# Performance work log

Measured on AMD Instinct MI355X. Metric: run time of the kernel, lower is better.

## Reference

```python
import jax, jax.numpy as jnp
import numpy as np

EMBED_DIM = 1024
HEAD_DIM = 64


def setup_inputs() -> dict:
    key = jax.random.key(0)
    ks = jax.random.split(key, 7)
    s_in = EMBED_DIM ** -0.5  # torch Linear default init scale
    x = jax.random.normal(ks[0], (4, 4096, EMBED_DIM), dtype=jnp.float32)
    Wk = jax.random.uniform(ks[1], (HEAD_DIM, EMBED_DIM), jnp.float32, -s_in, s_in)
    bk = jax.random.uniform(ks[2], (HEAD_DIM,), jnp.float32, -s_in, s_in)
    Wq = jax.random.uniform(ks[3], (HEAD_DIM, EMBED_DIM), jnp.float32, -s_in, s_in)
    bq = jax.random.uniform(ks[4], (HEAD_DIM,), jnp.float32, -s_in, s_in)
    Wv = jax.random.uniform(ks[5], (HEAD_DIM, EMBED_DIM), jnp.float32, -s_in, s_in)
    bv = jax.random.uniform(ks[6], (HEAD_DIM,), jnp.float32, -s_in, s_in)
    return {"x": x, "Wq": Wq, "bq": bq, "Wk": Wk, "bk": bk, "Wv": Wv, "bv": bv}


def reference(x, Wq, bq, Wk, bk, Wv, bv):
    # torch Linear: y = x @ W.T + b
    q = jnp.einsum('btc,dc->btd', x, Wq) + bq  # [B,T,D]
    k = jnp.einsum('btc,dc->btd', x, Wk) + bk
    v = jnp.einsum('btc,dc->btd', x, Wv) + bv
    scale = HEAD_DIM ** -0.5
    # NOTE: original divides by scale (multiplies by sqrt(head_dim)) -- faithful
    scores = jnp.einsum('btd,bsd->bts', q, k) / scale  # [B,T,T]
    attn_weights = jax.nn.softmax(scores, axis=-1)
    return jnp.einsum('bts,bsd->btd', attn_weights, v)
```

## Files before the change

kernel.cpp:

```cpp
#include <hip/hip_runtime.h>

#define BATCH 4
#define SEQ   4096
#define CDIM  1024
#define DDIM  64
#define NROW  (BATCH * SEQ)
#define SPA   70
#define NSPL  8

typedef _Float16 f16;
typedef _Float16 f16x8 __attribute__((ext_vector_type(8)));
typedef _Float16 f16x4 __attribute__((ext_vector_type(4)));
typedef __fp16   h16x2 __attribute__((ext_vector_type(2)));
typedef float    f32x4 __attribute__((ext_vector_type(4)));

#define MFMA32(a, b, c) __builtin_amdgcn_mfma_f32_16x16x32_f16((a), (b), (c), 0, 0, 0)
#define MFMA16(a, b, c) __builtin_amdgcn_mfma_f32_16x16x16f16((a), (b), (c), 0, 0, 0)

#define GLDS(g, l)                                                            \
  __builtin_amdgcn_global_load_lds((const __attribute__((address_space(1))) void*)(g), \
                                   (__attribute__((address_space(3))) void*)(l), 16, 0, 0)

#define QSCALE 11.5415603f

__device__ inline f16x8 cvt8(f32x4 a, f32x4 b) {
  h16x2 p0 = __builtin_amdgcn_cvt_pkrtz(a[0], a[1]);
  h16x2 p1 = __builtin_amdgcn_cvt_pkrtz(a[2], a[3]);
  h16x2 p2 = __builtin_amdgcn_cvt_pkrtz(b[0], b[1]);
  h16x2 p3 = __builtin_amdgcn_cvt_pkrtz(b[2], b[3]);
  f16x8 r;
  r[0] = p0[0]; r[1] = p0[1]; r[2] = p1[0]; r[3] = p1[1];
  r[4] = p2[0]; r[5] = p2[1]; r[6] = p3[0]; r[7] = p3[1];
  return r;
}

__device__ inline f16x4 cvt4(float a, float b, float c, float d) {
  h16x2 lo = __builtin_amdgcn_cvt_pkrtz(a, b);
  h16x2 hi = __builtin_amdgcn_cvt_pkrtz(c, d);
  f16x4 r;
  r[0] = lo[0]; r[1] = lo[1]; r[2] = hi[0]; r[3] = hi[1];
  return r;
}

__global__ __launch_bounds__(256) void prep_w_kernel(const float* __restrict__ Wq,
                                                     const float* __restrict__ Wk,
                                                     const float* __restrict__ Wv,
                                                     f16* __restrict__ wf2) {
  const int t = blockIdx.x * 256 + threadIdx.x;
  const int lane = t & 63;
  const int s = t >> 6;
  const int mt = s % 12, ck = s / 12;
  const int mat = mt >> 2, tile = mt & 3;
  const int n = lane & 15, quad = lane >> 4;
  const float* W = (mat == 0) ? Wq : (mat == 1) ? Wk : Wv;
  const float* src = W + (size_t)(tile * 16 + n) * CDIM + ck * 32 + quad * 8;
  const f32x4 a = *(const f32x4*)src;
  const f32x4 b = *(const f32x4*)(src + 4);
  *(f16x8*)(wf2 + (size_t)t * 8) = cvt8(a, b);
}

__global__ __launch_bounds__(256, 2) void proj_kernel(const float* __restrict__ x,
                                                      const f16* __restrict__ wf2,
                                                      const float* __restrict__ bq,
                                                      const float* __restrict__ bk,
                                                      const float* __restrict__ bv,
                                                      f16* __restrict__ qs,
                                                      f16* __restrict__ ks,
                                                      f16* __restrict__ vT) {
  __shared__ __attribute__((aligned(16))) char smem[2 * 16384];
  const int tid = threadIdx.x, lane = tid & 63, w = tid >> 6;
  const int n = lane & 15, quad = lane >> 4;
  const int rowbase = blockIdx.x * 32;

  const float* xsl = x + (size_t)(rowbase + w * 8 + (lane >> 3)) * CDIM + (lane & 7) * 4;
  const f16* wsl[3];
#pragma unroll
  for (int i = 0; i < 3; ++i)
    wsl[i] = wf2 + (size_t)(w * 3 + i) * 512 + lane * 8;

  f32x4 acc[2][3];
#pragma unroll
  for (int g = 0; g < 2; ++g)
#pragma unroll
    for (int i = 0; i < 3; ++i) acc[g][i] = (f32x4){0.f, 0.f, 0.f, 0.f};

  auto issue = [&](int ck, int b) {
    char* base = smem + b * 16384;
    GLDS(xsl + ck * 32, base + w * 1024);
#pragma unroll
    for (int i = 0; i < 3; ++i)
      GLDS(wsl[i] + (size_t)ck * 12 * 512, base + 4096 + (w * 3 + i) * 1024);
  };

  issue(0, 0);
  __syncthreads();
  for (int ck = 0; ck < 32; ++ck) {
    const int b = ck & 1;
    if (ck + 1 < 32) issue(ck + 1, b ^ 1);
    const float* xb = (const float*)(smem + b * 16384);
    const f16* wb = (const f16*)(smem + b * 16384 + 4096);
    f16x8 a[2];
#pragma unroll
    for (int g = 0; g < 2; ++g) {
      const f32x4 x0 = *(const f32x4*)(xb + (g * 16 + n) * 32 + quad * 8);
      const f32x4 x1 = *(const f32x4*)(xb + (g * 16 + n) * 32 + quad * 8 + 4);
      a[g] = cvt8(x0, x1);
    }
#pragma unroll
    for (int i = 0; i < 3; ++i) {
      const f16x8 bf = *(const f16x8*)(wb + (w * 3 + i) * 512 + lane * 8);
      acc[0][i] = MFMA32(a[0], bf, acc[0][i]);
      acc[1][i] = MFMA32(a[1], bf, acc[1][i]);
    }
    __syncthreads();
  }

  const float* bias_p[3] = {bq, bk, bv};
#pragma unroll
  for (int i = 0; i < 3; ++i) {
    const int mt = w * 3 + i;
    const int mat = mt >> 2, tile = mt & 3;
    const int d = tile * 16 + n;
    const float bias = bias_p[mat][d];
#pragma unroll
    for (int g = 0; g < 2; ++g) {
      const int r0 = rowbase + g * 16 + quad * 4;
      f32x4 aa = acc[g][i];
      if (mat == 0) {
#pragma unroll
        for (int r = 0; r < 4; ++r)
          qs[(size_t)(r0 + r) * DDIM + d] = (f16)((aa[r] + bias) * QSCALE);
      } else if (mat == 1) {
#pragma unroll
        for (int r = 0; r < 4; ++r)
          ks[(size_t)(r0 + r) * DDIM + d] = (f16)(aa[r] + bias);
      } else {
        const int bb = r0 >> 12;
        const int t = r0 & (SEQ - 1);
        *(f16x4*)(vT + (size_t)(bb * 64 + d) * SEQ + t) =
            cvt4(aa[0] + bias, aa[1] + bias, aa[2] + bias, aa[3] + bias);
      }
    }
  }
}

template <int NSPLIT>
__global__ __launch_bounds__(256, 4) void attn_kernel(const f16* __restrict__ qs,
                                                      const f16* __restrict__ ks,
                                                      const f16* __restrict__ vT,
                                                      float* __restrict__ outp,
                                                      f16* __restrict__ pacc,
                                                      float* __restrict__ pm,
                                                      float* __restrict__ pl) {
  __shared__ __attribute__((aligned(16))) f16 lk[64][SPA];
  __shared__ __attribute__((aligned(16))) f16 lv[64][SPA];
  const int tid = threadIdx.x, lane = tid & 63, w = tid >> 6;
  const int n = lane & 15, quad = lane >> 4;
  const int split = blockIdx.x % NSPLIT;
  const int rowblk = blockIdx.x / NSPLIT;
  const int row0 = rowblk * 128 + w * 32;
  const int bb = row0 >> 12;
  const int kbase = split * (SEQ / NSPLIT);
  const int NC = SEQ / NSPLIT / 64;

  const f16* kb = ks + (size_t)bb * SEQ * DDIM;
  const f16* vb = vT + (size_t)bb * DDIM * SEQ;

  const int srow = tid >> 2;
  const int scol = (tid & 3) * 16;
  const f16* kgp = kb + (size_t)(kbase + srow) * DDIM + scol;
  const f16* vgp = vb + (size_t)srow * SEQ + kbase + scol;

  f16x8 qf[2][2];
#pragma unroll
  for (int g = 0; g < 2; ++g)
#pragma unroll
    for (int hh = 0; hh < 2; ++hh)
      qf[g][hh] = *(const f16x8*)(qs + (size_t)(row0 + g * 16 + n) * DDIM + hh * 32 + quad * 8);

  f32x4 acc[2][4];
  float m[2] = {-1e30f, -1e30f}, ll[2] = {0.f, 0.f};
#pragma unroll
  for (int g = 0; g < 2; ++g)
#pragma unroll
    for (int t = 0; t < 4; ++t) acc[g][t] = (f32x4){0.f, 0.f, 0.f, 0.f};

  f16x8 kr0, kr1, vr0, vr1;
  auto gload = [&](int c) {
    const f16* kp = kgp + (size_t)c * 64 * DDIM;
    kr0 = *(const f16x8*)kp;
    kr1 = *(const f16x8*)(kp + 8);
    const f16* vp = vgp + c * 64;
    vr0 = *(const f16x8*)vp;
    vr1 = *(const f16x8*)(vp + 8);
  };

  gload(0);
  for (int c = 0; c < NC; ++c) {
    *(f16x8*)&lk[srow][scol] = kr0;
    *(f16x8*)&lk[srow][scol + 8] = kr1;
    *(f16x8*)&lv[srow][scol] = vr0;
    *(f16x8*)&lv[srow][scol + 8] = vr1;
    __syncthreads();
    if (c + 1 < NC) gload(c + 1);

    f32x4 s[2][4];
#pragma unroll
    for (int st = 0; st < 4; ++st) {
      const f16x8 klo = *(const f16x8*)&lk[st * 16 + n][quad * 8];
      const f16x8 khi = *(const f16x8*)&lk[st * 16 + n][32 + quad * 8];
#pragma unroll
      for (int g = 0; g < 2; ++g) {
        f32x4 z = (f32x4){0.f, 0.f, 0.f, 0.f};
        z = MFMA32(klo, qf[g][0], z);
        s[g][st] = MFMA32(khi, qf[g][1], z);
      }
    }

    f16x4 pq[2][4];
#pragma unroll
    for (int g = 0; g < 2; ++g) {
      f32x4 mx;
#pragma unroll
      for (int r = 0; r < 4; ++r)
        mx[r] = fmaxf(fmaxf(s[g][0][r], s[g][1][r]), fmaxf(s[g][2][r], s[g][3][r]));
      float mloc = fmaxf(fmaxf(mx[0], mx[1]), fmaxf(mx[2], mx[3]));
      mloc = fmaxf(mloc, __shfl_xor(mloc, 16));
      mloc = fmaxf(mloc, __shfl_xor(mloc, 32));
      const float mnew = fmaxf(m[g], mloc);
      const float alpha = __builtin_amdgcn_exp2f(m[g] - mnew);
      m[g] = mnew;
      float psum = 0.f;
#pragma unroll
      for (int st = 0; st < 4; ++st) {
        f32x4 p;
#pragma unroll
        for (int r = 0; r < 4; ++r) p[r] = __builtin_amdgcn_exp2f(s[g][st][r] - mnew);
        psum += (p[0] + p[1]) + (p[2] + p[3]);
        pq[g][st] = cvt4(p[0], p[1], p[2], p[3]);
      }
      ll[g] = ll[g] * alpha + psum;
#pragma unroll
      for (int t = 0; t < 4; ++t) acc[g][t] *= alpha;
    }

#pragma unroll
    for (int t = 0; t < 4; ++t)
#pragma unroll
      for (int st = 0; st < 4; ++st) {
        const f16x4 va = *(const f16x4*)&lv[t * 16 + n][st * 16 + quad * 4];
        acc[0][t] = MFMA16(va, pq[0][st], acc[0][t]);
        acc[1][t] = MFMA16(va, pq[1][st], acc[1][t]);
      }
    __syncthreads();
  }

  float lred[2];
#pragma unroll
  for (int g = 0; g < 2; ++g) {
    float l = ll[g];
    l += __shfl_xor(l, 16);
    l += __shfl_xor(l, 32);
    lred[g] = l;
  }

  if (NSPLIT == 1) {
#pragma unroll
    for (int g = 0; g < 2; ++g) {
      const float inv = 1.0f / lred[g];
      const int q = row0 + g * 16 + n;
#pragma unroll
      for (int t = 0; t < 4; ++t) {
        f32x4 o = acc[g][t];
#pragma unroll
        for (int r = 0; r < 4; ++r) o[r] *= inv;
        *(f32x4*)(outp + (size_t)q * DDIM + t * 16 + quad * 4) = o;
      }
    }
  } else {
#pragma unroll
    for (int g = 0; g < 2; ++g) {
      const int q = row0 + g * 16 + n;
#pragma unroll
      for (int t = 0; t < 4; ++t)
        *(f16x4*)(pacc + ((size_t)split * NROW + q) * DDIM + t * 16 + quad * 4) =
            cvt4(acc[g][t][0], acc[g][t][1], acc[g][t][2], acc[g][t][3]);
      if (quad == 0) {
        pm[split * NROW + q] = m[g];
        pl[split * NROW + q] = lred[g];
      }
    }
  }
}

template <int NSPLIT>
__global__ __launch_bounds__(256) void combine_kernel(const f16* __restrict__ pacc,
                                                      const float* __restrict__ pm,
                                                      const float* __restrict__ pl,
                                                      float* __restrict__ out) {
  const int idx = blockIdx.x * 256 + threadIdx.x;
  const int row = idx >> 4;
  const int c = (idx & 15) * 4;
  float mm = pm[row];
#pragma unroll
  for (int s = 1; s < NSPLIT; ++s) mm = fmaxf(mm, pm[s * NROW + row]);
  float L = 0.f;
  f32x4 o = (f32x4){0.f, 0.f, 0.f, 0.f};
#pragma unroll
  for (int s = 0; s < NSPLIT; ++s) {
    const float e = __builtin_amdgcn_exp2f(pm[s * NROW + row] - mm);
    L += pl[s * NROW + row] * e;
    const f16x4 a = *(const f16x4*)(pacc + ((size_t)s * NROW + row) * DDIM + c);
#pragma unroll
    for (int j = 0; j < 4; ++j) o[j] += (float)a[j] * e;
  }
  const float inv = 1.0f / L;
#pragma unroll
  for (int j = 0; j < 4; ++j) o[j] *= inv;
  *(f32x4*)(out + (size_t)row * DDIM + c) = o;
}

extern "C" void kernel_launch(void* const* d_in, const int* in_sizes, int n_in,
                              void* d_out, int out_size, void* d_ws, size_t ws_size,
                              hipStream_t stream) {
  const float* x  = (const float*)d_in[0];
  const float* Wq = (const float*)d_in[1];
  const float* bq = (const float*)d_in[2];
  const float* Wk = (const float*)d_in[3];
  const float* bk = (const float*)d_in[4];
  const float* Wv = (const float*)d_in[5];
  const float* bv = (const float*)d_in[6];
  float* out = (float*)d_out;

  f16* wf2 = (f16*)d_ws;
  f16* qs = wf2 + 3 * 65536;
  f16* ks = qs + (size_t)NROW * DDIM;
  f16* vT = ks + (size_t)NROW * DDIM;
  f16* pacc = vT + (size_t)NROW * DDIM;
  float* pm = (float*)(pacc + (size_t)NSPL * NROW * DDIM);
  float* pl = pm + (size_t)NSPL * NROW;
  const size_t need = (size_t)((char*)(pl + (size_t)NSPL * NROW) - (char*)d_ws);

  prep_w_kernel<<<dim3(96), dim3(256), 0, stream>>>(Wq, Wk, Wv, wf2);
  proj_kernel<<<dim3(512), dim3(256), 0, stream>>>(x, wf2, bq, bk, bv, qs, ks, vT);

  if (ws_size >= need) {
    attn_kernel<NSPL><<<dim3(128 * NSPL), dim3(256), 0, stream>>>(qs, ks, vT, nullptr, pacc, pm, pl);
    combine_kernel<NSPL><<<dim3(NROW * 16 / 256), dim3(256), 0, stream>>>(pacc, pm, pl, out);
  } else {
    attn_kernel<1><<<dim3(128), dim3(256), 0, stream>>>(qs, ks, vT, out, nullptr, nullptr, nullptr);
  }
}
```

Before: 164.7 us.

## Swizzle K/V layouts and use async global-to-LDS double buffering in attention

The projection kernel now writes K with an XOR-swizzled column layout and V into per-64-key chunked, swizzled tiles, so the attention kernel can copy them straight into LDS with global_load_lds. It double-buffers the LDS tiles, drops the padded register-staged copy and one barrier per iteration, and reads through matching swizzles to avoid bank conflicts. The projection kernel also moves to 512 threads, with each wave doing one 16-row group and separate waves loading x versus weights. Together these raise LDS usage and rely on correct swizzle and index arithmetic across both kernels.

```diff
diff --git a/kernel.cpp b/kernel.cpp
--- a/kernel.cpp
+++ b/kernel.cpp
@@ -5,7 +5,6 @@
 #define CDIM  1024
 #define DDIM  64
 #define NROW  (BATCH * SEQ)
-#define SPA   70
 #define NSPL  8
 
 typedef _Float16 f16;
@@ -59,87 +58,86 @@
   *(f16x8*)(wf2 + (size_t)t * 8) = cvt8(a, b);
 }
 
-__global__ __launch_bounds__(256, 2) void proj_kernel(const float* __restrict__ x,
+__global__ __launch_bounds__(512, 4) void proj_kernel(const float* __restrict__ x,
                                                       const f16* __restrict__ wf2,
                                                       const float* __restrict__ bq,
                                                       const float* __restrict__ bk,
                                                       const float* __restrict__ bv,
                                                       f16* __restrict__ qs,
                                                       f16* __restrict__ ks,
-                                                      f16* __restrict__ vT) {
-  __shared__ __attribute__((aligned(16))) char smem[2 * 16384];
+                                                      f16* __restrict__ vc) {
+  __shared__ __attribute__((aligned(16))) char pbuf[2][16384];
   const int tid = threadIdx.x, lane = tid & 63, w = tid >> 6;
   const int n = lane & 15, quad = lane >> 4;
+  const int rw = w & 1, wc = w >> 1;
   const int rowbase = blockIdx.x * 32;
 
-  const float* xsl = x + (size_t)(rowbase + w * 8 + (lane >> 3)) * CDIM + (lane & 7) * 4;
-  const f16* wsl[3];
-#pragma unroll
-  for (int i = 0; i < 3; ++i)
-    wsl[i] = wf2 + (size_t)(w * 3 + i) * 512 + lane * 8;
-
-  f32x4 acc[2][3];
-#pragma unroll
-  for (int g = 0; g < 2; ++g)
-#pragma unroll
-    for (int i = 0; i < 3; ++i) acc[g][i] = (f32x4){0.f, 0.f, 0.f, 0.f};
-
-  auto issue = [&](int ck, int b) {
-    char* base = smem + b * 16384;
-    GLDS(xsl + ck * 32, base + w * 1024);
-#pragma unroll
-    for (int i = 0; i < 3; ++i)
-      GLDS(wsl[i] + (size_t)ck * 12 * 512, base + 4096 + (w * 3 + i) * 1024);
+  const int i0 = 2 * w;
+  const float* xs0 = x + (size_t)(rowbase + i0 * 8 + (lane >> 3)) * CDIM + (lane & 7) * 4;
+  const float* xs1 = xs0 + 8 * CDIM;
+  const int wi = (i0 >= 4) ? (i0 - 4) : 0;
+  const f16* ws0 = wf2 + (size_t)wi * 512 + lane * 8;
+  const f16* ws1 = ws0 + 512;
+
+  f32x4 acc[3];
+#pragma unroll
+  for (int i = 0; i < 3; ++i) acc[i] = (f32x4){0.f, 0.f, 0.f, 0.f};
+
+  auto issue = [&](int ck, int buf) {
+    char* base = &pbuf[buf][0];
+    if (i0 < 4) {
+      GLDS(xs0 + ck * 32, base + i0 * 1024);
+      GLDS(xs1 + ck * 32, base + (i0 + 1) * 1024);
+    } else {
+      GLDS(ws0 + (size_t)ck * 6144, base + 4096 + (i0 - 4) * 1024);
+      GLDS(ws1 + (size_t)ck * 6144, base + 4096 + (i0 - 3) * 1024);
+    }
   };
 
   issue(0, 0);
-  __syncthreads();
   for (int ck = 0; ck < 32; ++ck) {
     const int b = ck & 1;
+    __syncthreads();
     if (ck + 1 < 32) issue(ck + 1, b ^ 1);
-    const float* xb = (const float*)(smem + b * 16384);
-    const f16* wb = (const f16*)(smem + b * 16384 + 4096);
-    f16x8 a[2];
-#pragma unroll
-    for (int g = 0; g < 2; ++g) {
-      const f32x4 x0 = *(const f32x4*)(xb + (g * 16 + n) * 32 + quad * 8);
-      const f32x4 x1 = *(const f32x4*)(xb + (g * 16 + n) * 32 + quad * 8 + 4);
-      a[g] = cvt8(x0, x1);
-    }
+    const float* xb = (const float*)&pbuf[b][0];
+    const f16* wb = (const f16*)&pbuf[b][4096];
+    const f32x4 x0 = *(const f32x4*)(xb + (rw * 16 + n) * 32 + quad * 8);
+    const f32x4 x1 = *(const f32x4*)(xb + (rw * 16 + n) * 32 + quad * 8 + 4);
+    const f16x8 a = cvt8(x0, x1);
 #pragma unroll
     for (int i = 0; i < 3; ++i) {
-      const f16x8 bf = *(const f16x8*)(wb + (w * 3 + i) * 512 + lane * 8);
-      acc[0][i] = MFMA32(a[0], bf, acc[0][i]);
-      acc[1][i] = MFMA32(a[1], bf, acc[1][i]);
-    }
-    __syncthreads();
+      const f16x8 bf = *(const f16x8*)(wb + (wc * 3 + i) * 512 + lane * 8);
+      acc[i] = MFMA32(a, bf, acc[i]);
+    }
   }
 
   const float* bias_p[3] = {bq, bk, bv};
 #pragma unroll
   for (int i = 0; i < 3; ++i) {
-    const int mt = w * 3 + i;
+    const int mt = wc * 3 + i;
     const int mat = mt >> 2, tile = mt & 3;
     const int d = tile * 16 + n;
     const float bias = bias_p[mat][d];
-#pragma unroll
-    for (int g = 0; g < 2; ++g) {
-      const int r0 = rowbase + g * 16 + quad * 4;
-      f32x4 aa = acc[g][i];
-      if (mat == 0) {
-#pragma unroll
-        for (int r = 0; r < 4; ++r)
-          qs[(size_t)(r0 + r) * DDIM + d] = (f16)((aa[r] + bias) * QSCALE);
-      } else if (mat == 1) {
-#pragma unroll
-        for (int r = 0; r < 4; ++r)
-          ks[(size_t)(r0 + r) * DDIM + d] = (f16)(aa[r] + bias);
-      } else {
-        const int bb = r0 >> 12;
-        const int t = r0 & (SEQ - 1);
-        *(f16x4*)(vT + (size_t)(bb * 64 + d) * SEQ + t) =
-            cvt4(aa[0] + bias, aa[1] + bias, aa[2] + bias, aa[3] + bias);
-      }
+    const int r0 = rowbase + rw * 16 + quad * 4;
+    const f32x4 aa = acc[i];
+    if (mat == 0) {
+#pragma unroll
+      for (int r = 0; r < 4; ++r)
+        qs[(size_t)(r0 + r) * DDIM + d] = (f16)((aa[r] + bias) * QSCALE);
+    } else if (mat == 1) {
+#pragma unroll
+      for (int r = 0; r < 4; ++r) {
+        const int t = r0 + r;
+        const int col = ((((d >> 3) ^ (t & 7)) << 3) | (n & 7));
+        ks[(size_t)t * DDIM + col] = (f16)(aa[r] + bias);
+      }
+    } else {
+      const int bb = r0 >> 12;
+      const int tl = r0 & (SEQ - 1);
+      const int ck2 = tl >> 6;
+      const int bsw = (((tl & 63) >> 2) ^ n) << 2;
+      *(f16x4*)(vc + ((size_t)(bb * 64 + ck2) * 64 + d) * 64 + bsw) =
+          cvt4(aa[0] + bias, aa[1] + bias, aa[2] + bias, aa[3] + bias);
     }
   }
 }
@@ -147,13 +145,13 @@
 template <int NSPLIT>
 __global__ __launch_bounds__(256, 4) void attn_kernel(const f16* __restrict__ qs,
                                                       const f16* __restrict__ ks,
-                                                      const f16* __restrict__ vT,
+                                                      const f16* __restrict__ vc,
                                                       float* __restrict__ outp,
                                                       f16* __restrict__ pacc,
                                                       float* __restrict__ pm,
                                                       float* __restrict__ pl) {
-  __shared__ __attribute__((aligned(16))) f16 lk[64][SPA];
-  __shared__ __attribute__((aligned(16))) f16 lv[64][SPA];
+  __shared__ __attribute__((aligned(16))) f16 lk[2][4096];
+  __shared__ __attribute__((aligned(16))) f16 lv[2][4096];
   const int tid = threadIdx.x, lane = tid & 63, w = tid >> 6;
   const int n = lane & 15, quad = lane >> 4;
   const int split = blockIdx.x % NSPLIT;
@@ -161,15 +159,20 @@
   const int row0 = rowblk * 128 + w * 32;
   const int bb = row0 >> 12;
   const int kbase = split * (SEQ / NSPLIT);
+  const int kc0 = kbase >> 6;
   const int NC = SEQ / NSPLIT / 64;
 
-  const f16* kb = ks + (size_t)bb * SEQ * DDIM;
-  const f16* vb = vT + (size_t)bb * DDIM * SEQ;
-
-  const int srow = tid >> 2;
-  const int scol = (tid & 3) * 16;
-  const f16* kgp = kb + (size_t)(kbase + srow) * DDIM + scol;
-  const f16* vgp = vb + (size_t)srow * SEQ + kbase + scol;
+  const f16* ksb = ks + (size_t)bb * SEQ * DDIM;
+  const f16* vcb = vc + (size_t)bb * 64 * 4096;
+
+  auto issue = [&](int c, int buf) {
+#pragma unroll
+    for (int i = 0; i < 2; ++i) {
+      const int id = 2 * w + i;
+      GLDS(ksb + (size_t)(kbase + c * 64) * 64 + id * 512 + lane * 8, &lk[buf][id * 512]);
+      GLDS(vcb + (size_t)(kc0 + c) * 4096 + id * 512 + lane * 8, &lv[buf][id * 512]);
+    }
+  };
 
   f16x8 qf[2][2];
 #pragma unroll
@@ -178,6 +181,11 @@
     for (int hh = 0; hh < 2; ++hh)
       qf[g][hh] = *(const f16x8*)(qs + (size_t)(row0 + g * 16 + n) * DDIM + hh * 32 + quad * 8);
 
+  const int kswz = (quad ^ (n & 7)) << 3;
+  int vswz[4];
+#pragma unroll
+  for (int st = 0; st < 4; ++st) vswz[st] = ((((st << 2) | quad) ^ n) << 2);
+
   f32x4 acc[2][4];
   float m[2] = {-1e30f, -1e30f}, ll[2] = {0.f, 0.f};
 #pragma unroll
@@ -185,30 +193,18 @@
 #pragma unroll
     for (int t = 0; t < 4; ++t) acc[g][t] = (f32x4){0.f, 0.f, 0.f, 0.f};
 
-  f16x8 kr0, kr1, vr0, vr1;
-  auto gload = [&](int c) {
-    const f16* kp = kgp + (size_t)c * 64 * DDIM;
-    kr0 = *(const f16x8*)kp;
-    kr1 = *(const f16x8*)(kp + 8);
-    const f16* vp = vgp + c * 64;
-    vr0 = *(const f16x8*)vp;
-    vr1 = *(const f16x8*)(vp + 8);
-  };
-
-  gload(0);
+  issue(0, 0);
   for (int c = 0; c < NC; ++c) {
-    *(f16x8*)&lk[srow][scol] = kr0;
-    *(f16x8*)&lk[srow][scol + 8] = kr1;
-    *(f16x8*)&lv[srow][scol] = vr0;
-    *(f16x8*)&lv[srow][scol + 8] = vr1;
+    const int b = c & 1;
     __syncthreads();
-    if (c + 1 < NC) gload(c + 1);
+    if (c + 1 < NC) issue(c + 1, b ^ 1);
 
     f32x4 s[2][4];
 #pragma unroll
     for (int st = 0; st < 4; ++st) {
-      const f16x8 klo = *(const f16x8*)&lk[st * 16 + n][quad * 8];
-      const f16x8 khi = *(const f16x8*)&lk[st * 16 + n][32 + quad * 8];
+      const f16* lkr = &lk[b][(st * 16 + n) * 64];
+      const f16x8 klo = *(const f16x8*)(lkr + kswz);
+      const f16x8 khi = *(const f16x8*)(lkr + (kswz ^ 32));
 #pragma unroll
       for (int g = 0; g < 2; ++g) {
         f32x4 z = (f32x4){0.f, 0.f, 0.f, 0.f};
@@ -245,14 +241,15 @@
     }
 
 #pragma unroll
-    for (int t = 0; t < 4; ++t)
+    for (int dt = 0; dt < 4; ++dt) {
+      const f16* lvr = &lv[b][(dt * 16 + n) * 64];
 #pragma unroll
       for (int st = 0; st < 4; ++st) {
-        const f16x4 va = *(const f16x4*)&lv[t * 16 + n][st * 16 + quad * 4];
-        acc[0][t] = MFMA16(va, pq[0][st], acc[0][t]);
-        acc[1][t] = MFMA16(va, pq[1][st], acc[1][t]);
-      }
-    __syncthreads();
+        const f16x4 va = *(const f16x4*)(lvr + vswz[st]);
+        acc[0][dt] = MFMA16(va, pq[0][st], acc[0][dt]);
+        acc[1][dt] = MFMA16(va, pq[1][st], acc[1][dt]);
+      }
+    }
   }
 
   float lred[2];
@@ -335,19 +332,19 @@
   f16* wf2 = (f16*)d_ws;
   f16* qs = wf2 + 3 * 65536;
   f16* ks = qs + (size_t)NROW * DDIM;
-  f16* vT = ks + (size_t)NROW * DDIM;
-  f16* pacc = vT + (size_t)NROW * DDIM;
+  f16* vc = ks + (size_t)NROW * DDIM;
+  f16* pacc = vc + (size_t)NROW * DDIM;
   float* pm = (float*)(pacc + (size_t)NSPL * NROW * DDIM);
   float* pl = pm + (size_t)NSPL * NROW;
   const size_t need = (size_t)((char*)(pl + (size_t)NSPL * NROW) - (char*)d_ws);
 
   prep_w_kernel<<<dim3(96), dim3(256), 0, stream>>>(Wq, Wk, Wv, wf2);
-  proj_kernel<<<dim3(512), dim3(256), 0, stream>>>(x, wf2, bq, bk, bv, qs, ks, vT);
+  proj_kernel<<<dim3(512), dim3(512), 0, stream>>>(x, wf2, bq, bk, bv, qs, ks, vc);
 
   if (ws_size >= need) {
-    attn_kernel<NSPL><<<dim3(128 * NSPL), dim3(256), 0, stream>>>(qs, ks, vT, nullptr, pacc, pm, pl);
+    attn_kernel<NSPL><<<dim3(128 * NSPL), dim3(256), 0, stream>>>(qs, ks, vc, nullptr, pacc, pm, pl);
     combine_kernel<NSPL><<<dim3(NROW * 16 / 256), dim3(256), 0, stream>>>(pacc, pm, pl, out);
   } else {
-    attn_kernel<1><<<dim3(128), dim3(256), 0, stream>>>(qs, ks, vT, out, nullptr, nullptr, nullptr);
-  }
-}
+    attn_kernel<1><<<dim3(128), dim3(256), 0, stream>>>(qs, ks, vc, out, nullptr, nullptr, nullptr);
+  }
+}
```

After: 161.8 us. About the same (-1.7%).
